# Kernel optimization log

Hardware: AMD Instinct MI355X
Metric: run time of the kernel (lower is better)

## Reference

```python
import jax, jax.numpy as jnp
import numpy as np

EPS = 1e-6      # torch F.pairwise_distance default eps (added to the difference)
MARGIN = 1.0

def _cdist_eps(a, b):
    # Exact ||a_i - b_j + eps||_2 via expansion:
    # ||a-b+eps||^2 = ||a||^2 + ||b||^2 - 2 a.b + 2*eps*(sum(a)-sum(b)) + D*eps^2
    D = a.shape[-1]
    sq = (jnp.sum(a * a, axis=1)[:, None]
          + jnp.sum(b * b, axis=1)[None, :]
          - 2.0 * (a @ b.T)
          + 2.0 * EPS * (jnp.sum(a, axis=1)[:, None] - jnp.sum(b, axis=1)[None, :])
          + D * EPS * EPS)
    return jnp.sqrt(jnp.maximum(sq, 0.0))

def setup_inputs() -> dict:
    key = jax.random.key(0)
    k1, k2, k3 = jax.random.split(key, 3)
    B, D = 4096, 1024
    return {
        'anchor_embeddings': jax.random.normal(k1, (B, D), dtype=jnp.float32),
        'positive_embeddings': jax.random.normal(k2, (B, D), dtype=jnp.float32),
        'negative_embeddings': jax.random.normal(k3, (B, D), dtype=jnp.float32),
    }

def reference(anchor_embeddings, positive_embeddings, negative_embeddings):
    a, p, n = anchor_embeddings, positive_embeddings, negative_embeddings
    # per-row anchor-positive and anchor-negative distances
    d_ap = jnp.linalg.norm(a - p + EPS, axis=-1)          # [B]
    d_an_row = jnp.linalg.norm(a - n + EPS, axis=-1)      # [B]

    # hardest negative: for each anchor, max over negatives with dist < d_ap[i], else 0
    dan_mat = _cdist_eps(a, n)                            # [B, B]
    mask_n = dan_mat < d_ap[:, None]
    hard_n = jnp.where(mask_n.any(axis=1),
                       jnp.max(jnp.where(mask_n, dan_mat, -jnp.inf), axis=1),
                       0.0)
    d_an = jnp.mean(hard_n)                               # scalar

    # hardest positive: for each anchor, min over positives with dist > d(a_i, n_i), else 0
    dpp_mat = _cdist_eps(a, p)                            # [B, B]
    mask_p = dpp_mat > d_an_row[:, None]
    hard_p = jnp.where(mask_p.any(axis=1),
                       jnp.min(jnp.where(mask_p, dpp_mat, jnp.inf), axis=1),
                       0.0)
    d_pp = jnp.mean(hard_p)                               # scalar

    loss = jnp.mean(jnp.clip(d_ap - 0.5 * d_pp - 0.5 * d_an + MARGIN, 0.0, None))
    return loss
```

## Files before the change

### kernel.cpp

```cpp
#include <hip/hip_runtime.h>


#define NB 4096
#define DIM 1024
#define EPSF 1e-6f
#define D_EPS2 (1024.0f * 1e-6f * 1e-6f)

#define BM 128
#define BK 64

typedef __bf16  bf16x8 __attribute__((ext_vector_type(8)));
typedef float   f32x4  __attribute__((ext_vector_type(4)));

__device__ __forceinline__ unsigned short f2bf(float x) {
    unsigned u = __float_as_uint(x);
    u += 0x7FFFu + ((u >> 16) & 1u);
    return (unsigned short)(u >> 16);
}

__device__ __forceinline__ void g2l16(const unsigned short* g, unsigned short* l) {
    __builtin_amdgcn_global_load_lds(
        (const __attribute__((address_space(1))) unsigned int*)g,
        (__attribute__((address_space(3))) unsigned int*)l, 16, 0, 0);
}


__global__ __launch_bounds__(256) void row_stats_kernel(
    const float* __restrict__ a, const float* __restrict__ p,
    const float* __restrict__ n,
    unsigned short* __restrict__ abf, unsigned short* __restrict__ pbf,
    unsigned short* __restrict__ nbf, float* __restrict__ stats)
{
    const int t    = threadIdx.x;
    const int wave = t >> 6, lane = t & 63;
    const int row  = blockIdx.x * 4 + wave;
    const size_t base = (size_t)row * DIM;

    const float4* a4 = (const float4*)(a + base);
    const float4* p4 = (const float4*)(p + base);
    const float4* n4 = (const float4*)(n + base);

    float v[8] = {0,0,0,0,0,0,0,0};
#pragma unroll
    for (int c = 0; c < 4; c++) {
        const int idx = c * 64 + lane;
        const float4 va = a4[idx];
        const float4 vp = p4[idx];
        const float4 vn = n4[idx];
        const float fa[4] = {va.x, va.y, va.z, va.w};
        const float fp[4] = {vp.x, vp.y, vp.z, vp.w};
        const float fn[4] = {vn.x, vn.y, vn.z, vn.w};
#pragma unroll
        for (int e = 0; e < 4; e++) {
            v[0] += fa[e];           v[1] += fa[e] * fa[e];
            v[2] += fp[e];           v[3] += fp[e] * fp[e];
            v[4] += fn[e];           v[5] += fn[e] * fn[e];
            float dp = fa[e] - fp[e] + EPSF;  v[6] += dp * dp;
            float dn = fa[e] - fn[e] + EPSF;  v[7] += dn * dn;
        }
        ushort4 ba, bp, bn;
        ba.x = f2bf(fa[0]); ba.y = f2bf(fa[1]); ba.z = f2bf(fa[2]); ba.w = f2bf(fa[3]);
        bp.x = f2bf(fp[0]); bp.y = f2bf(fp[1]); bp.z = f2bf(fp[2]); bp.w = f2bf(fp[3]);
        bn.x = f2bf(fn[0]); bn.y = f2bf(fn[1]); bn.z = f2bf(fn[2]); bn.w = f2bf(fn[3]);
        ((ushort4*)(abf + base))[idx] = ba;
        ((ushort4*)(pbf + base))[idx] = bp;
        ((ushort4*)(nbf + base))[idx] = bn;
    }

#pragma unroll
    for (int m = 32; m >= 1; m >>= 1)
#pragma unroll
        for (int q = 0; q < 8; q++) v[q] += __shfl_xor(v[q], m);

    if (lane == 0) {
        stats[0 * NB + row] = v[1] + 2.0f * EPSF * v[0] + D_EPS2;
        stats[1 * NB + row] = v[5] - 2.0f * EPSF * v[4];
        stats[2 * NB + row] = v[3] - 2.0f * EPSF * v[2];
        stats[3 * NB + row] = sqrtf(v[6]);
        stats[4 * NB + row] = sqrtf(v[7]);
        ((unsigned*)stats)[5 * NB + row] = 0u;
        ((unsigned*)stats)[6 * NB + row] = 0x7f800000u;
    }
}

__global__ __launch_bounds__(256, 2) void gemm_mask_kernel(
    const unsigned short* __restrict__ Abf,
    const unsigned short* __restrict__ Nbf,
    const unsigned short* __restrict__ Pbf,
    float* __restrict__ stats)
{
    const int i0 = blockIdx.x * BM;
    const int j0 = blockIdx.y * BM;

    __shared__ unsigned short sA[BM * BK];
    __shared__ unsigned short sN[BM * BK];
    __shared__ unsigned short sP[BM * BK];

    const int t    = threadIdx.x;
    const int wave = t >> 6, lane = t & 63;
    const int wm   = wave >> 1, wn = wave & 1;
    const int quad = lane >> 4, lrow = lane & 15;

    const int srow = lane >> 3;
    const int kch  = ((lane & 7) ^ srow) * 8;
    const unsigned short* gA = Abf + (size_t)(i0 + wave * 32 + srow) * DIM + kch;
    const unsigned short* gN = Nbf + (size_t)(j0 + wave * 32 + srow) * DIM + kch;
    const unsigned short* gP = Pbf + (size_t)(j0 + wave * 32 + srow) * DIM + kch;
    unsigned short* lA = sA + (wave * 32) * BK;
    unsigned short* lN = sN + (wave * 32) * BK;
    unsigned short* lP = sP + (wave * 32) * BK;

    const int rsw0 = ((0 * 4 + quad) ^ (lrow & 7)) * 8;
    const int rsw1 = ((1 * 4 + quad) ^ (lrow & 7)) * 8;
    const unsigned short* pa  = sA + (wm * 64 + lrow) * BK;
    const unsigned short* pbn = sN + (wn * 64 + lrow) * BK;
    const unsigned short* pbp = sP + (wn * 64 + lrow) * BK;

    f32x4 accN[4][4], accP[4][4];
#pragma unroll
    for (int im = 0; im < 4; im++)
#pragma unroll
        for (int jn = 0; jn < 4; jn++) {
            accN[im][jn] = (f32x4)(0.0f);
            accP[im][jn] = (f32x4)(0.0f);
        }

    for (int kt = 0; kt < DIM; kt += BK) {
        __syncthreads();
#pragma unroll
        for (int g = 0; g < 4; g++) {
            g2l16(gA + (size_t)kt + g * 8 * DIM, lA + g * 8 * BK);
            g2l16(gN + (size_t)kt + g * 8 * DIM, lN + g * 8 * BK);
            g2l16(gP + (size_t)kt + g * 8 * DIM, lP + g * 8 * BK);
        }
        __syncthreads();

#pragma unroll
        for (int half = 0; half < 2; half++) {
            const int rsw = half ? rsw1 : rsw0;
            bf16x8 afr[4], bn_fr[4], bp_fr[4];
#pragma unroll
            for (int im = 0; im < 4; im++)
                afr[im] = *(const bf16x8*)(pa + im * 16 * BK + rsw);
#pragma unroll
            for (int jn = 0; jn < 4; jn++) {
                bn_fr[jn] = *(const bf16x8*)(pbn + jn * 16 * BK + rsw);
                bp_fr[jn] = *(const bf16x8*)(pbp + jn * 16 * BK + rsw);
            }
#pragma unroll
            for (int im = 0; im < 4; im++)
#pragma unroll
                for (int jn = 0; jn < 4; jn++) {
                    accN[im][jn] = __builtin_amdgcn_mfma_f32_16x16x32_bf16(
                        afr[im], bn_fr[jn], accN[im][jn], 0, 0, 0);
                    accP[im][jn] = __builtin_amdgcn_mfma_f32_16x16x32_bf16(
                        afr[im], bp_fr[jn], accP[im][jn], 0, 0, 0);
                }
        }
    }

    const float* __restrict__ base_a = stats + 0 * NB;
    const float* __restrict__ cn_v   = stats + 1 * NB;
    const float* __restrict__ cp_v   = stats + 2 * NB;
    const float* __restrict__ d_ap   = stats + 3 * NB;
    const float* __restrict__ d_an   = stats + 4 * NB;
    unsigned* __restrict__ hard_n = ((unsigned*)stats) + 5 * NB;
    unsigned* __restrict__ hard_p = ((unsigned*)stats) + 6 * NB;

#pragma unroll
    for (int im = 0; im < 4; im++) {
#pragma unroll
        for (int r = 0; r < 4; r++) {
            const int gi = i0 + wm * 64 + im * 16 + quad * 4 + r;
            const float cutN = d_ap[gi];
            const float cutP = d_an[gi];
            const float bi   = base_a[gi];
            float bestN = 0.0f;
            float bestP = __uint_as_float(0x7f800000u);
#pragma unroll
            for (int jn = 0; jn < 4; jn++) {
                const int gj = j0 + wn * 64 + jn * 16 + lrow;
                const float dN = sqrtf(fmaxf(bi + cn_v[gj] - 2.0f * accN[im][jn][r], 0.0f));
                const float dP = sqrtf(fmaxf(bi + cp_v[gj] - 2.0f * accP[im][jn][r], 0.0f));
                if (dN < cutN && dN > bestN) bestN = dN;
                if (dP > cutP && dP < bestP) bestP = dP;
            }
#pragma unroll
            for (int m = 1; m < 16; m <<= 1) {
                bestN = fmaxf(bestN, __shfl_xor(bestN, m));
                bestP = fminf(bestP, __shfl_xor(bestP, m));
            }
            if (lrow == 0) {
                const unsigned bn_ = __float_as_uint(bestN);
                const unsigned bp_ = __float_as_uint(bestP);
                if (bn_ != 0u)          atomicMax(hard_n + gi, bn_);
                if (bp_ != 0x7f800000u) atomicMin(hard_p + gi, bp_);
            }
        }
    }
}

__global__ __launch_bounds__(1024) void finalize_kernel(
    const float* __restrict__ stats, float* __restrict__ out)
{
    const unsigned* hard_n = ((const unsigned*)stats) + 5 * NB;
    const unsigned* hard_p = ((const unsigned*)stats) + 6 * NB;
    const float*    d_ap   = stats + 3 * NB;
    const int t = threadIdx.x;
    const int wave = t >> 6, lane = t & 63;
    __shared__ float pn[16], pp[16];
    __shared__ float s_dan, s_dpp;

    float sn = 0.0f, sp = 0.0f;
    for (int i = t; i < NB; i += 1024) {
        sn += __uint_as_float(hard_n[i]);
        const unsigned hp = hard_p[i];
        if (hp != 0x7f800000u) sp += __uint_as_float(hp);
    }
#pragma unroll
    for (int m = 32; m >= 1; m >>= 1) {
        sn += __shfl_xor(sn, m);
        sp += __shfl_xor(sp, m);
    }
    if (lane == 0) { pn[wave] = sn; pp[wave] = sp; }
    __syncthreads();
    if (t == 0) {
        float an = 0.0f, ap = 0.0f;
#pragma unroll
        for (int w = 0; w < 16; w++) { an += pn[w]; ap += pp[w]; }
        s_dan = an / (float)NB;
        s_dpp = ap / (float)NB;
    }
    __syncthreads();
    const float dan = s_dan, dpp = s_dpp;

    float accv = 0.0f;
    for (int i = t; i < NB; i += 1024)
        accv += fmaxf(d_ap[i] - 0.5f * dpp - 0.5f * dan + 1.0f, 0.0f);
#pragma unroll
    for (int m = 32; m >= 1; m >>= 1) accv += __shfl_xor(accv, m);
    if (lane == 0) pn[wave] = accv;
    __syncthreads();
    if (t == 0) {
        float s = 0.0f;
#pragma unroll
        for (int w = 0; w < 16; w++) s += pn[w];
        out[0] = s / (float)NB;
    }
}

extern "C" void kernel_launch(void* const* d_in, const int* in_sizes, int n_in,
                              void* d_out, int out_size, void* d_ws, size_t ws_size,
                              hipStream_t stream) {
    const float* a = (const float*)d_in[0];
    const float* p = (const float*)d_in[1];
    const float* n = (const float*)d_in[2];
    float* out = (float*)d_out;

    unsigned short* abf = (unsigned short*)d_ws;
    unsigned short* pbf = abf + (size_t)NB * DIM;
    unsigned short* nbf = pbf + (size_t)NB * DIM;
    float* stats = (float*)(nbf + (size_t)NB * DIM);

    row_stats_kernel<<<NB / 4, 256, 0, stream>>>(a, p, n, abf, pbf, nbf, stats);

    dim3 grid(NB / BM, NB / BM);
    gemm_mask_kernel<<<grid, 256, 0, stream>>>(abf, nbf, pbf, stats);

    finalize_kernel<<<1, 1024, 0, stream>>>(stats, out);
}
```

Measured before the change: 183.6 us.

## Double-buffer LDS and enlarge GEMM tile to 256x128 with 8 waves

Moves the fused dual-GEMM kernel to 512-thread blocks over a 256x128 tile, with double-buffered LDS for the A, N and P slices. The next k-slice's global-to-LDS loads are issued while MFMAs run on the current buffer. The MFMA phases are split into four sub-phases with barriers and s_setprio so loads and compute interleave. This aims to hide global load latency and cut per-tile reloads of B. In exchange it doubles LDS use (about 128KB per block), which may limit occupancy, and adds many barriers.

```diff
diff --git a/kernel.cpp b/kernel.cpp
--- a/kernel.cpp
+++ b/kernel.cpp
@@ -6,7 +6,8 @@
 #define EPSF 1e-6f
 #define D_EPS2 (1024.0f * 1e-6f * 1e-6f)
 
-#define BM 128
+#define BM 256
+#define BN 128
 #define BK 64
 
 typedef __bf16  bf16x8 __attribute__((ext_vector_type(8)));
@@ -83,38 +84,36 @@
     }
 }
 
-__global__ __launch_bounds__(256, 2) void gemm_mask_kernel(
+__global__ __launch_bounds__(512, 2) void gemm_mask_kernel(
     const unsigned short* __restrict__ Abf,
     const unsigned short* __restrict__ Nbf,
     const unsigned short* __restrict__ Pbf,
     float* __restrict__ stats)
 {
     const int i0 = blockIdx.x * BM;
-    const int j0 = blockIdx.y * BM;
-
-    __shared__ unsigned short sA[BM * BK];
-    __shared__ unsigned short sN[BM * BK];
-    __shared__ unsigned short sP[BM * BK];
+    const int j0 = blockIdx.y * BN;
+
+    __shared__ unsigned short sA[2][BM * BK];
+    __shared__ unsigned short sN[2][BN * BK];
+    __shared__ unsigned short sP[2][BN * BK];
 
     const int t    = threadIdx.x;
     const int wave = t >> 6, lane = t & 63;
     const int wm   = wave >> 1, wn = wave & 1;
     const int quad = lane >> 4, lrow = lane & 15;
 
-    const int srow = lane >> 3;
-    const int kch  = ((lane & 7) ^ srow) * 8;
-    const unsigned short* gA = Abf + (size_t)(i0 + wave * 32 + srow) * DIM + kch;
-    const unsigned short* gN = Nbf + (size_t)(j0 + wave * 32 + srow) * DIM + kch;
-    const unsigned short* gP = Pbf + (size_t)(j0 + wave * 32 + srow) * DIM + kch;
-    unsigned short* lA = sA + (wave * 32) * BK;
-    unsigned short* lN = sN + (wave * 32) * BK;
-    unsigned short* lP = sP + (wave * 32) * BK;
-
-    const int rsw0 = ((0 * 4 + quad) ^ (lrow & 7)) * 8;
-    const int rsw1 = ((1 * 4 + quad) ^ (lrow & 7)) * 8;
-    const unsigned short* pa  = sA + (wm * 64 + lrow) * BK;
-    const unsigned short* pbn = sN + (wn * 64 + lrow) * BK;
-    const unsigned short* pbp = sP + (wn * 64 + lrow) * BK;
+    const int srow = t >> 3;
+    const int slot = t & 7;
+    const int kch  = (slot ^ (srow & 7)) * 8;
+    const unsigned short* gA = Abf + (size_t)(i0 + srow) * DIM + kch;
+    const unsigned short* gN = Nbf + (size_t)(j0 + srow) * DIM + kch;
+    const unsigned short* gP = Pbf + (size_t)(j0 + srow) * DIM + kch;
+    const int lofs = srow * BK + slot * 8;
+
+    const int aoff = (wm * 64 + lrow) * BK;
+    const int boff = (wn * 64 + lrow) * BK;
+    const int rk0  = ((0 + quad) ^ (lrow & 7)) * 8;
+    const int rk1  = ((4 + quad) ^ (lrow & 7)) * 8;
 
     f32x4 accN[4][4], accP[4][4];
 #pragma unroll
@@ -125,39 +124,98 @@
             accP[im][jn] = (f32x4)(0.0f);
         }
 
-    for (int kt = 0; kt < DIM; kt += BK) {
-        __syncthreads();
-#pragma unroll
-        for (int g = 0; g < 4; g++) {
-            g2l16(gA + (size_t)kt + g * 8 * DIM, lA + g * 8 * BK);
-            g2l16(gN + (size_t)kt + g * 8 * DIM, lN + g * 8 * BK);
-            g2l16(gP + (size_t)kt + g * 8 * DIM, lP + g * 8 * BK);
-        }
-        __syncthreads();
-
-#pragma unroll
-        for (int half = 0; half < 2; half++) {
-            const int rsw = half ? rsw1 : rsw0;
-            bf16x8 afr[4], bn_fr[4], bp_fr[4];
-#pragma unroll
-            for (int im = 0; im < 4; im++)
-                afr[im] = *(const bf16x8*)(pa + im * 16 * BK + rsw);
-#pragma unroll
-            for (int jn = 0; jn < 4; jn++) {
-                bn_fr[jn] = *(const bf16x8*)(pbn + jn * 16 * BK + rsw);
-                bp_fr[jn] = *(const bf16x8*)(pbp + jn * 16 * BK + rsw);
-            }
-#pragma unroll
-            for (int im = 0; im < 4; im++)
-#pragma unroll
-                for (int jn = 0; jn < 4; jn++) {
-                    accN[im][jn] = __builtin_amdgcn_mfma_f32_16x16x32_bf16(
-                        afr[im], bn_fr[jn], accN[im][jn], 0, 0, 0);
-                    accP[im][jn] = __builtin_amdgcn_mfma_f32_16x16x32_bf16(
-                        afr[im], bp_fr[jn], accP[im][jn], 0, 0, 0);
-                }
-        }
-    }
+#define STAGE_A(NBUF, KTN)                                                    \
+    _Pragma("unroll")                                                         \
+    for (int g = 0; g < 4; g++)                                               \
+        g2l16(gA + (size_t)(KTN) + (size_t)(g * 64) * DIM,                    \
+              &sA[NBUF][(g * 64) * BK + lofs]);
+
+#define STAGE_NP(NBUF, KTN)                                                   \
+    _Pragma("unroll")                                                         \
+    for (int g = 0; g < 2; g++) {                                             \
+        g2l16(gN + (size_t)(KTN) + (size_t)(g * 64) * DIM,                    \
+              &sN[NBUF][(g * 64) * BK + lofs]);                               \
+        g2l16(gP + (size_t)(KTN) + (size_t)(g * 64) * DIM,                    \
+              &sP[NBUF][(g * 64) * BK + lofs]);                               \
+    }
+
+#define MFMA16(ACC, AF, BF)                                                   \
+    _Pragma("unroll")                                                         \
+    for (int im = 0; im < 4; im++)                                            \
+        _Pragma("unroll")                                                     \
+        for (int jn = 0; jn < 4; jn++)                                        \
+            ACC[im][jn] = __builtin_amdgcn_mfma_f32_16x16x32_bf16(            \
+                AF[im], BF[jn], ACC[im][jn], 0, 0, 0);
+
+#define TILE(B, NBUF, KTN, DO_STAGE)                                          \
+  {                                                                           \
+    bf16x8 af0[4], af1[4], bfr[4];                                            \
+                                       \
+    _Pragma("unroll")                                                         \
+    for (int im = 0; im < 4; im++)                                            \
+        af0[im] = *(const bf16x8*)&sA[B][aoff + im * 16 * BK + rk0];          \
+    _Pragma("unroll")                                                         \
+    for (int jn = 0; jn < 4; jn++)                                            \
+        bfr[jn] = *(const bf16x8*)&sN[B][boff + jn * 16 * BK + rk0];          \
+    if (DO_STAGE) { STAGE_A(NBUF, KTN); }                                     \
+    __builtin_amdgcn_s_barrier();                                             \
+    asm volatile("s_waitcnt lgkmcnt(0)" ::: "memory");                        \
+    __builtin_amdgcn_s_setprio(1);                                            \
+    MFMA16(accN, af0, bfr);                                                   \
+    __builtin_amdgcn_s_setprio(0);                                            \
+    __builtin_amdgcn_s_barrier();                                             \
+                                     \
+    _Pragma("unroll")                                                         \
+    for (int im = 0; im < 4; im++)                                            \
+        af1[im] = *(const bf16x8*)&sA[B][aoff + im * 16 * BK + rk1];          \
+    _Pragma("unroll")                                                         \
+    for (int jn = 0; jn < 4; jn++)                                            \
+        bfr[jn] = *(const bf16x8*)&sN[B][boff + jn * 16 * BK + rk1];          \
+    if (DO_STAGE) { STAGE_NP(NBUF, KTN); }                                    \
+    __builtin_amdgcn_s_barrier();                                             \
+    asm volatile("s_waitcnt lgkmcnt(0)" ::: "memory");                        \
+    __builtin_amdgcn_s_setprio(1);                                            \
+    MFMA16(accN, af1, bfr);                                                   \
+    __builtin_amdgcn_s_setprio(0);                                            \
+    __builtin_amdgcn_s_barrier();                                             \
+                                                      \
+    _Pragma("unroll")                                                         \
+    for (int jn = 0; jn < 4; jn++)                                            \
+        bfr[jn] = *(const bf16x8*)&sP[B][boff + jn * 16 * BK + rk0];          \
+    __builtin_amdgcn_s_barrier();                                             \
+    asm volatile("s_waitcnt lgkmcnt(0)" ::: "memory");                        \
+    __builtin_amdgcn_s_setprio(1);                                            \
+    MFMA16(accP, af0, bfr);                                                   \
+    __builtin_amdgcn_s_setprio(0);                                            \
+    __builtin_amdgcn_s_barrier();                                             \
+         \
+    _Pragma("unroll")                                                         \
+    for (int jn = 0; jn < 4; jn++)                                            \
+        bfr[jn] = *(const bf16x8*)&sP[B][boff + jn * 16 * BK + rk1];          \
+    __builtin_amdgcn_s_barrier();                                             \
+    asm volatile("s_waitcnt lgkmcnt(0)" ::: "memory");                        \
+    __builtin_amdgcn_s_setprio(1);                                            \
+    MFMA16(accP, af1, bfr);                                                   \
+    __builtin_amdgcn_s_setprio(0);                                            \
+    asm volatile("s_waitcnt vmcnt(0)" ::: "memory");                          \
+    __builtin_amdgcn_s_barrier();                                             \
+  }
+
+    STAGE_A(0, 0);
+    STAGE_NP(0, 0);
+    asm volatile("s_waitcnt vmcnt(0)" ::: "memory");
+    __builtin_amdgcn_s_barrier();
+
+#pragma unroll 1
+    for (int kt = 0; kt < DIM; kt += 2 * BK) {
+        TILE(0, 1, kt + BK, 1);
+        TILE(1, 0, kt + 2 * BK, (kt + 2 * BK) < DIM);
+    }
+
+#undef TILE
+#undef MFMA16
+#undef STAGE_NP
+#undef STAGE_A
 
     const float* __restrict__ base_a = stats + 0 * NB;
     const float* __restrict__ cn_v   = stats + 1 * NB;
@@ -264,8 +322,8 @@
 
     row_stats_kernel<<<NB / 4, 256, 0, stream>>>(a, p, n, abf, pbf, nbf, stats);
 
-    dim3 grid(NB / BM, NB / BM);
-    gemm_mask_kernel<<<grid, 256, 0, stream>>>(abf, nbf, pbf, stats);
+    dim3 grid(NB / BM, NB / BN);
+    gemm_mask_kernel<<<grid, 512, 0, stream>>>(abf, nbf, pbf, stats);
 
     finalize_kernel<<<1, 1024, 0, stream>>>(stats, out);
 }
```

Result: no change. 184.7 us (+0.6%).

## Split fused N/P GEMM into separate blocks with swizzled 1D grid

Applied to the files above, without the earlier changes.

Each block now computes only one of the anchor-negative or anchor-positive distance tiles instead of both, halving the accumulators, LDS usage and B-operand loads per block. This lets the launch bound rise to three blocks per CU. The grid becomes a flat 2048-block launch with an XCD-style swizzle that maps consecutive blocks onto tiles. The trade-off is that the A tile is now loaded twice, once by the N block and once by the P block, and each block does less MFMA work per A load.

```diff
diff --git a/kernel.cpp b/kernel.cpp
--- a/kernel.cpp
+++ b/kernel.cpp
@@ -83,18 +83,23 @@
     }
 }
 
-__global__ __launch_bounds__(256, 2) void gemm_mask_kernel(
+__global__ __launch_bounds__(256, 3) void gemm_mask_kernel(
     const unsigned short* __restrict__ Abf,
     const unsigned short* __restrict__ Nbf,
     const unsigned short* __restrict__ Pbf,
     float* __restrict__ stats)
 {
-    const int i0 = blockIdx.x * BM;
-    const int j0 = blockIdx.y * BM;
+    const int flat = (int)blockIdx.x;
+    const int swz  = (flat & 7) * 256 + (flat >> 3);
+    const int bz   = swz >> 10;
+    const int rem  = swz & 1023;
+    const int i0   = (rem & 31) * BM;
+    const int j0   = (rem >> 5) * BM;
+
+    const unsigned short* __restrict__ Bbf = bz ? Pbf : Nbf;
 
     __shared__ unsigned short sA[BM * BK];
-    __shared__ unsigned short sN[BM * BK];
-    __shared__ unsigned short sP[BM * BK];
+    __shared__ unsigned short sB[BM * BK];
 
     const int t    = threadIdx.x;
     const int wave = t >> 6, lane = t & 63;
@@ -104,97 +109,92 @@
     const int srow = lane >> 3;
     const int kch  = ((lane & 7) ^ srow) * 8;
     const unsigned short* gA = Abf + (size_t)(i0 + wave * 32 + srow) * DIM + kch;
-    const unsigned short* gN = Nbf + (size_t)(j0 + wave * 32 + srow) * DIM + kch;
-    const unsigned short* gP = Pbf + (size_t)(j0 + wave * 32 + srow) * DIM + kch;
+    const unsigned short* gB = Bbf + (size_t)(j0 + wave * 32 + srow) * DIM + kch;
     unsigned short* lA = sA + (wave * 32) * BK;
-    unsigned short* lN = sN + (wave * 32) * BK;
-    unsigned short* lP = sP + (wave * 32) * BK;
+    unsigned short* lB = sB + (wave * 32) * BK;
 
     const int rsw0 = ((0 * 4 + quad) ^ (lrow & 7)) * 8;
     const int rsw1 = ((1 * 4 + quad) ^ (lrow & 7)) * 8;
-    const unsigned short* pa  = sA + (wm * 64 + lrow) * BK;
-    const unsigned short* pbn = sN + (wn * 64 + lrow) * BK;
-    const unsigned short* pbp = sP + (wn * 64 + lrow) * BK;
-
-    f32x4 accN[4][4], accP[4][4];
+    const unsigned short* pa = sA + (wm * 64 + lrow) * BK;
+    const unsigned short* pb = sB + (wn * 64 + lrow) * BK;
+
+    f32x4 acc[4][4];
 #pragma unroll
     for (int im = 0; im < 4; im++)
 #pragma unroll
-        for (int jn = 0; jn < 4; jn++) {
-            accN[im][jn] = (f32x4)(0.0f);
-            accP[im][jn] = (f32x4)(0.0f);
-        }
+        for (int jn = 0; jn < 4; jn++)
+            acc[im][jn] = (f32x4)(0.0f);
 
     for (int kt = 0; kt < DIM; kt += BK) {
         __syncthreads();
 #pragma unroll
         for (int g = 0; g < 4; g++) {
             g2l16(gA + (size_t)kt + g * 8 * DIM, lA + g * 8 * BK);
-            g2l16(gN + (size_t)kt + g * 8 * DIM, lN + g * 8 * BK);
-            g2l16(gP + (size_t)kt + g * 8 * DIM, lP + g * 8 * BK);
+            g2l16(gB + (size_t)kt + g * 8 * DIM, lB + g * 8 * BK);
         }
         __syncthreads();
 
 #pragma unroll
         for (int half = 0; half < 2; half++) {
             const int rsw = half ? rsw1 : rsw0;
-            bf16x8 afr[4], bn_fr[4], bp_fr[4];
+            bf16x8 afr[4], bfr[4];
 #pragma unroll
             for (int im = 0; im < 4; im++)
                 afr[im] = *(const bf16x8*)(pa + im * 16 * BK + rsw);
 #pragma unroll
-            for (int jn = 0; jn < 4; jn++) {
-                bn_fr[jn] = *(const bf16x8*)(pbn + jn * 16 * BK + rsw);
-                bp_fr[jn] = *(const bf16x8*)(pbp + jn * 16 * BK + rsw);
-            }
+            for (int jn = 0; jn < 4; jn++)
+                bfr[jn] = *(const bf16x8*)(pb + jn * 16 * BK + rsw);
 #pragma unroll
             for (int im = 0; im < 4; im++)
 #pragma unroll
-                for (int jn = 0; jn < 4; jn++) {
-                    accN[im][jn] = __builtin_amdgcn_mfma_f32_16x16x32_bf16(
-                        afr[im], bn_fr[jn], accN[im][jn], 0, 0, 0);
-                    accP[im][jn] = __builtin_amdgcn_mfma_f32_16x16x32_bf16(
-                        afr[im], bp_fr[jn], accP[im][jn], 0, 0, 0);
-                }
+                for (int jn = 0; jn < 4; jn++)
+                    acc[im][jn] = __builtin_amdgcn_mfma_f32_16x16x32_bf16(
+                        afr[im], bfr[jn], acc[im][jn], 0, 0, 0);
         }
     }
 
     const float* __restrict__ base_a = stats + 0 * NB;
-    const float* __restrict__ cn_v   = stats + 1 * NB;
-    const float* __restrict__ cp_v   = stats + 2 * NB;
-    const float* __restrict__ d_ap   = stats + 3 * NB;
-    const float* __restrict__ d_an   = stats + 4 * NB;
-    unsigned* __restrict__ hard_n = ((unsigned*)stats) + 5 * NB;
-    unsigned* __restrict__ hard_p = ((unsigned*)stats) + 6 * NB;
+    const float* __restrict__ cv     = stats + (bz ? 2 : 1) * NB;
+    const float* __restrict__ cut_v  = stats + (bz ? 4 : 3) * NB;
+    unsigned* __restrict__ hard = ((unsigned*)stats) + (bz ? 6 : 5) * NB;
 
 #pragma unroll
     for (int im = 0; im < 4; im++) {
 #pragma unroll
         for (int r = 0; r < 4; r++) {
             const int gi = i0 + wm * 64 + im * 16 + quad * 4 + r;
-            const float cutN = d_ap[gi];
-            const float cutP = d_an[gi];
-            const float bi   = base_a[gi];
-            float bestN = 0.0f;
-            float bestP = __uint_as_float(0x7f800000u);
-#pragma unroll
-            for (int jn = 0; jn < 4; jn++) {
-                const int gj = j0 + wn * 64 + jn * 16 + lrow;
-                const float dN = sqrtf(fmaxf(bi + cn_v[gj] - 2.0f * accN[im][jn][r], 0.0f));
-                const float dP = sqrtf(fmaxf(bi + cp_v[gj] - 2.0f * accP[im][jn][r], 0.0f));
-                if (dN < cutN && dN > bestN) bestN = dN;
-                if (dP > cutP && dP < bestP) bestP = dP;
-            }
-#pragma unroll
-            for (int m = 1; m < 16; m <<= 1) {
-                bestN = fmaxf(bestN, __shfl_xor(bestN, m));
-                bestP = fminf(bestP, __shfl_xor(bestP, m));
-            }
-            if (lrow == 0) {
-                const unsigned bn_ = __float_as_uint(bestN);
-                const unsigned bp_ = __float_as_uint(bestP);
-                if (bn_ != 0u)          atomicMax(hard_n + gi, bn_);
-                if (bp_ != 0x7f800000u) atomicMin(hard_p + gi, bp_);
+            const float cut = cut_v[gi];
+            const float bi  = base_a[gi];
+            if (bz == 0) {
+                float best = 0.0f;
+#pragma unroll
+                for (int jn = 0; jn < 4; jn++) {
+                    const int gj = j0 + wn * 64 + jn * 16 + lrow;
+                    const float d = sqrtf(fmaxf(bi + cv[gj] - 2.0f * acc[im][jn][r], 0.0f));
+                    if (d < cut && d > best) best = d;
+                }
+#pragma unroll
+                for (int m = 1; m < 16; m <<= 1)
+                    best = fmaxf(best, __shfl_xor(best, m));
+                if (lrow == 0) {
+                    const unsigned b_ = __float_as_uint(best);
+                    if (b_ != 0u) atomicMax(hard + gi, b_);
+                }
+            } else {
+                float best = __uint_as_float(0x7f800000u);
+#pragma unroll
+                for (int jn = 0; jn < 4; jn++) {
+                    const int gj = j0 + wn * 64 + jn * 16 + lrow;
+                    const float d = sqrtf(fmaxf(bi + cv[gj] - 2.0f * acc[im][jn][r], 0.0f));
+                    if (d > cut && d < best) best = d;
+                }
+#pragma unroll
+                for (int m = 1; m < 16; m <<= 1)
+                    best = fminf(best, __shfl_xor(best, m));
+                if (lrow == 0) {
+                    const unsigned b_ = __float_as_uint(best);
+                    if (b_ != 0x7f800000u) atomicMin(hard + gi, b_);
+                }
             }
         }
     }
@@ -264,8 +264,7 @@
 
     row_stats_kernel<<<NB / 4, 256, 0, stream>>>(a, p, n, abf, pbf, nbf, stats);
 
-    dim3 grid(NB / BM, NB / BM);
-    gemm_mask_kernel<<<grid, 256, 0, stream>>>(abf, nbf, pbf, stats);
+    gemm_mask_kernel<<<2048, 256, 0, stream>>>(abf, nbf, pbf, stats);
 
     finalize_kernel<<<1, 1024, 0, stream>>>(stats, out);
 }
```

Result: no change. 185.9 us (+1.3%).

## Load anchor fragments directly from global into registers, drop sA LDS tile

Applied to the files above, without the earlier changes.

The anchor tile is no longer staged through shared memory. Each wave now loads its A MFMA fragments straight from global memory into registers, with the second K-half prefetched while the first half's MFMAs issue. This frees a third of the LDS and cuts LDS traffic, and launch bounds are raised from 2 to 3 blocks per SM to use the freed space. In exchange, A is loaded redundantly by the two wn waves through the cache, and the tighter register budget from the higher occupancy target may cause spills with 32 accumulator vectors.

```diff
diff --git a/kernel.cpp b/kernel.cpp
--- a/kernel.cpp
+++ b/kernel.cpp
@@ -83,7 +83,7 @@
     }
 }
 
-__global__ __launch_bounds__(256, 2) void gemm_mask_kernel(
+__global__ __launch_bounds__(256, 3) void gemm_mask_kernel(
     const unsigned short* __restrict__ Abf,
     const unsigned short* __restrict__ Nbf,
     const unsigned short* __restrict__ Pbf,
@@ -92,7 +92,6 @@
     const int i0 = blockIdx.x * BM;
     const int j0 = blockIdx.y * BM;
 
-    __shared__ unsigned short sA[BM * BK];
     __shared__ unsigned short sN[BM * BK];
     __shared__ unsigned short sP[BM * BK];
 
@@ -103,16 +102,16 @@
 
     const int srow = lane >> 3;
     const int kch  = ((lane & 7) ^ srow) * 8;
-    const unsigned short* gA = Abf + (size_t)(i0 + wave * 32 + srow) * DIM + kch;
     const unsigned short* gN = Nbf + (size_t)(j0 + wave * 32 + srow) * DIM + kch;
     const unsigned short* gP = Pbf + (size_t)(j0 + wave * 32 + srow) * DIM + kch;
-    unsigned short* lA = sA + (wave * 32) * BK;
     unsigned short* lN = sN + (wave * 32) * BK;
     unsigned short* lP = sP + (wave * 32) * BK;
 
+    const unsigned short* aBase =
+        Abf + (size_t)(i0 + wm * 64 + lrow) * DIM + quad * 8;
+
     const int rsw0 = ((0 * 4 + quad) ^ (lrow & 7)) * 8;
     const int rsw1 = ((1 * 4 + quad) ^ (lrow & 7)) * 8;
-    const unsigned short* pa  = sA + (wm * 64 + lrow) * BK;
     const unsigned short* pbn = sN + (wn * 64 + lrow) * BK;
     const unsigned short* pbp = sP + (wn * 64 + lrow) * BK;
 
@@ -129,34 +128,49 @@
         __syncthreads();
 #pragma unroll
         for (int g = 0; g < 4; g++) {
-            g2l16(gA + (size_t)kt + g * 8 * DIM, lA + g * 8 * BK);
             g2l16(gN + (size_t)kt + g * 8 * DIM, lN + g * 8 * BK);
             g2l16(gP + (size_t)kt + g * 8 * DIM, lP + g * 8 * BK);
         }
+        bf16x8 af0[4];
+#pragma unroll
+        for (int im = 0; im < 4; im++)
+            af0[im] = *(const bf16x8*)(aBase + (size_t)im * 16 * DIM + kt);
         __syncthreads();
 
-#pragma unroll
-        for (int half = 0; half < 2; half++) {
-            const int rsw = half ? rsw1 : rsw0;
-            bf16x8 afr[4], bn_fr[4], bp_fr[4];
-#pragma unroll
-            for (int im = 0; im < 4; im++)
-                afr[im] = *(const bf16x8*)(pa + im * 16 * BK + rsw);
+        bf16x8 bn_fr[4], bp_fr[4];
+#pragma unroll
+        for (int jn = 0; jn < 4; jn++) {
+            bn_fr[jn] = *(const bf16x8*)(pbn + jn * 16 * BK + rsw0);
+            bp_fr[jn] = *(const bf16x8*)(pbp + jn * 16 * BK + rsw0);
+        }
+        bf16x8 af1[4];
+#pragma unroll
+        for (int im = 0; im < 4; im++)
+            af1[im] = *(const bf16x8*)(aBase + (size_t)im * 16 * DIM + kt + 32);
+#pragma unroll
+        for (int im = 0; im < 4; im++)
 #pragma unroll
             for (int jn = 0; jn < 4; jn++) {
-                bn_fr[jn] = *(const bf16x8*)(pbn + jn * 16 * BK + rsw);
-                bp_fr[jn] = *(const bf16x8*)(pbp + jn * 16 * BK + rsw);
-            }
-#pragma unroll
-            for (int im = 0; im < 4; im++)
-#pragma unroll
-                for (int jn = 0; jn < 4; jn++) {
-                    accN[im][jn] = __builtin_amdgcn_mfma_f32_16x16x32_bf16(
-                        afr[im], bn_fr[jn], accN[im][jn], 0, 0, 0);
-                    accP[im][jn] = __builtin_amdgcn_mfma_f32_16x16x32_bf16(
-                        afr[im], bp_fr[jn], accP[im][jn], 0, 0, 0);
-                }
-        }
+                accN[im][jn] = __builtin_amdgcn_mfma_f32_16x16x32_bf16(
+                    af0[im], bn_fr[jn], accN[im][jn], 0, 0, 0);
+                accP[im][jn] = __builtin_amdgcn_mfma_f32_16x16x32_bf16(
+                    af0[im], bp_fr[jn], accP[im][jn], 0, 0, 0);
+            }
+
+#pragma unroll
+        for (int jn = 0; jn < 4; jn++) {
+            bn_fr[jn] = *(const bf16x8*)(pbn + jn * 16 * BK + rsw1);
+            bp_fr[jn] = *(const bf16x8*)(pbp + jn * 16 * BK + rsw1);
+        }
+#pragma unroll
+        for (int im = 0; im < 4; im++)
+#pragma unroll
+            for (int jn = 0; jn < 4; jn++) {
+                accN[im][jn] = __builtin_amdgcn_mfma_f32_16x16x32_bf16(
+                    af1[im], bn_fr[jn], accN[im][jn], 0, 0, 0);
+                accP[im][jn] = __builtin_amdgcn_mfma_f32_16x16x32_bf16(
+                    af1[im], bp_fr[jn], accP[im][jn], 0, 0, 0);
+            }
     }
 
     const float* __restrict__ base_a = stats + 0 * NB;
```

Result: slower. 373.7 us (+103.6%).
